# Optimization experiments

Measured on AMD Instinct MI355X. Metric: run time of the kernel, lower is better.

The kernel has to match this reference:

```python
import jax, jax.numpy as jnp
import numpy as np

D_MODEL = 1024
HEAD_SIZE = 128
SCALE = float(np.sqrt(HEAD_SIZE))


def setup_inputs() -> dict:
    key = jax.random.key(0)
    kx, kq, kk, kv = jax.random.split(key, 4)
    B, T = 4, 4096
    x = jax.random.normal(kx, (B, T, D_MODEL), dtype=jnp.float32)
    # torch nn.Linear(d_model, head_size, bias=False) weight: [head_size, d_model]
    s = 1.0 / np.sqrt(D_MODEL)
    Wq = jax.random.uniform(kq, (HEAD_SIZE, D_MODEL), jnp.float32, -s, s)
    Wk = jax.random.uniform(kk, (HEAD_SIZE, D_MODEL), jnp.float32, -s, s)
    Wv = jax.random.uniform(kv, (HEAD_SIZE, D_MODEL), jnp.float32, -s, s)
    return {"x": x, "Wq": Wq, "Wk": Wk, "Wv": Wv}


def reference(x, Wq, Wk, Wv):
    B, T, C = x.shape
    q = jnp.einsum('btc,hc->bth', x, Wq)  # [B,T,hs]
    k = jnp.einsum('btc,hc->bth', x, Wk)
    v = jnp.einsum('btc,hc->bth', x, Wv)
    scores = jnp.einsum('bth,bsh->bts', q, k) / SCALE  # [B,T,T]
    causal = jnp.tril(jnp.ones((T, T), dtype=bool))
    scores = jnp.where(causal, scores, -jnp.inf)
    attn = jax.nn.softmax(scores, axis=-1)
    # dropout p=0.0 -> identity
    return jnp.einsum('bts,bsh->bth', attn, v)
```

## Files before the change

kernel.cpp:

```cpp
#include <hip/hip_runtime.h>


typedef __attribute__((ext_vector_type(8))) short short8;
typedef __attribute__((ext_vector_type(8))) unsigned short ushort8;
typedef __attribute__((ext_vector_type(4))) unsigned short ushort4v;
typedef __attribute__((ext_vector_type(4))) float f32x4;
typedef __attribute__((ext_vector_type(16))) float f32x16;
typedef __attribute__((ext_vector_type(4))) int int4v;
typedef unsigned int u32;
typedef unsigned short u16;

#define MFMA32(a, b, c) __builtin_amdgcn_mfma_f32_32x32x16_bf16((a), (b), (c), 0, 0, 0)
#define WAITVM0() asm volatile("s_waitcnt vmcnt(0)" ::: "memory")
#define NEG_INF (-1e30f)

__device__ __forceinline__ void gload16(const void* g, void* l) {
  __builtin_amdgcn_global_load_lds((const __attribute__((address_space(1))) u32*)g,
                                   (__attribute__((address_space(3))) u32*)l, 16, 0, 0);
}

__device__ __forceinline__ u16 f2bf(float f) {
  u32 u = __builtin_bit_cast(u32, f);
  u = u + 0x7FFFu + ((u >> 16) & 1u);
  return (u16)(u >> 16);
}

__device__ __forceinline__ u32 cvtpk(float lo, float hi) {
  u32 r;
  asm("v_cvt_pk_bf16_f32 %0, %1, %2" : "=v"(r) : "v"(lo), "v"(hi));
  return r;
}

__global__ __launch_bounds__(256) void wconv_kernel(const float* __restrict__ Wq,
                                                    const float* __restrict__ Wk,
                                                    const float* __restrict__ Wv,
                                                    u16* __restrict__ Wb) {
  int g = (blockIdx.x * 256 + threadIdx.x) * 8;
  const float* src;
  if (g < 131072)      src = Wq + g;
  else if (g < 262144) src = Wk + (g - 131072);
  else                 src = Wv + (g - 262144);
  float4 a = *(const float4*)src;
  float4 b = *(const float4*)(src + 4);
  ushort8 o;
  o[0] = f2bf(a.x); o[1] = f2bf(a.y); o[2] = f2bf(a.z); o[3] = f2bf(a.w);
  o[4] = f2bf(b.x); o[5] = f2bf(b.y); o[6] = f2bf(b.z); o[7] = f2bf(b.w);
  *(ushort8*)(Wb + g) = o;
}

#define QK_SCALE 0.127517446f

__global__ __launch_bounds__(512, 2) void qkv_proj_kernel(const float* __restrict__ x,
                                                          const u16* __restrict__ Wb,
                                                          u16* __restrict__ qout,
                                                          u16* __restrict__ kout,
                                                          u16* __restrict__ vtout) {
  __shared__ __align__(16) unsigned char Wlds[2][49152];
  __shared__ __align__(16) unsigned char Xlds[2][8192];
  const int tid = threadIdx.x;
  const int w = tid >> 6;
  const int l = tid & 63;
  const int h = l >> 5, n32 = l & 31;
  const int mh = w >> 2, ng = w & 3;
  const int m0 = (int)blockIdx.x * 64;

  const int xr = tid >> 3, xc = tid & 7;
  const float* xsrc = x + (size_t)(m0 + xr) * 1024 + xc * 8;
  unsigned char* const xw0 = (unsigned char*)Xlds[0] + xr * 128 + ((xc * 16) ^ ((xr & 7) << 4));
  unsigned char* const xw1 = (unsigned char*)Xlds[1] + xr * 128 + ((xc * 16) ^ ((xr & 7) << 4));

  f32x16 acc[3];
#pragma unroll
  for (int j = 0; j < 3; ++j)
#pragma unroll
    for (int r = 0; r < 16; ++r) acc[j][r] = 0.f;

#define STAGE_W(buf, ks)                                                       \
  {                                                                            \
    _Pragma("unroll") for (int c = 0; c < 6; ++c) {                            \
      int L = c * 512 + tid;                                                   \
      int row = L >> 3, chp = L & 7;                                           \
      int gch = chp ^ (row & 7);                                               \
      gload16((const char*)Wb + row * 2048 + (ks) * 128 + gch * 16,            \
              (unsigned char*)Wlds[buf] + c * 8192 + w * 1024);                \
    }                                                                          \
  }

  float4 xa = *(const float4*)(xsrc);
  float4 xb = *(const float4*)(xsrc + 4);
  STAGE_W(0, 0);

  const int am = mh * 32 + n32;
  const int asw = (am & 7) << 4;
  int cur = 0;

  for (int ks = 0; ks < 16; ++ks) {
    int4v xv;
    xv[0] = (int)cvtpk(xa.x, xa.y);
    xv[1] = (int)cvtpk(xa.z, xa.w);
    xv[2] = (int)cvtpk(xb.x, xb.y);
    xv[3] = (int)cvtpk(xb.z, xb.w);
    *(int4v*)(cur ? xw1 : xw0) = xv;
    __syncthreads();
    if (ks < 15) {
      xa = *(const float4*)(xsrc + (ks + 1) * 64);
      xb = *(const float4*)(xsrc + (ks + 1) * 64 + 4);
      STAGE_W(cur ^ 1, ks + 1);
    }
    const char* xb0 = (const char*)Xlds[cur];
    const char* wb0 = (const char*)Wlds[cur];
    __builtin_amdgcn_s_setprio(1);
#pragma unroll
    for (int k16 = 0; k16 < 4; ++k16) {
      short8 a = *(const short8*)(xb0 + am * 128 + ((k16 * 32 + h * 16) ^ asw));
#pragma unroll
      for (int j = 0; j < 3; ++j) {
        int nrow = (ng * 3 + j) * 32 + n32;
        short8 b = *(const short8*)(wb0 + nrow * 128 +
                                    ((k16 * 32 + h * 16) ^ ((nrow & 7) << 4)));
        acc[j] = MFMA32(a, b, acc[j]);
      }
    }
    __builtin_amdgcn_s_setprio(0);
    cur ^= 1;
  }
#undef STAGE_W

  const int m0e = m0 + mh * 32;
#pragma unroll
  for (int j = 0; j < 3; ++j) {
    int ti = ng * 3 + j;
    int gcol = ti * 32 + n32;
    if (ti < 4) {
#pragma unroll
      for (int r = 0; r < 16; ++r) {
        int row = m0e + (r & 3) + 8 * (r >> 2) + 4 * h;
        qout[(size_t)row * 128 + gcol] = f2bf(acc[j][r] * QK_SCALE);
      }
    } else if (ti < 8) {
#pragma unroll
      for (int r = 0; r < 16; ++r) {
        int row = m0e + (r & 3) + 8 * (r >> 2) + 4 * h;
        kout[(size_t)row * 128 + (gcol - 128)] = f2bf(acc[j][r]);
      }
    } else {
      int d = gcol - 256;
#pragma unroll
      for (int rq = 0; rq < 4; ++rq) {
        int t0 = m0e + rq * 8 + 4 * h;
        ushort4v o4;
#pragma unroll
        for (int i = 0; i < 4; ++i) o4[i] = f2bf(acc[j][rq * 4 + i]);
        *(ushort4v*)&vtout[(size_t)((t0 >> 12) * 128 + d) * 4096 + (t0 & 4095)] = o4;
      }
    }
  }
}

template <int NSPLIT>
__global__ __launch_bounds__(256, 2) void attn_kernel(const u16* __restrict__ qws,
                                                      const u16* __restrict__ kws,
                                                      const u16* __restrict__ vtws,
                                                      float* __restrict__ out,
                                                      float* __restrict__ opart,
                                                      float* __restrict__ mlpart) {
  __shared__ __align__(16) unsigned char Klds[2][16384];
  __shared__ __align__(16) unsigned char Vlds[2][16384];

  const int tid = threadIdx.x;
  const int w = tid >> 6;
  const int l = tid & 63;
  const int h = l >> 5, q32 = l & 31;
  const int bid = (int)blockIdx.x;
  const int sp = bid & (NSPLIT - 1);
  const int tb = bid / NSPLIT;
  const int bi = tb & 3;
  const int qt = 31 - (tb >> 2);
  const int q0w = qt * 128 + w * 32;
  const int grow = bi * 4096 + q0w + q32;
  const int qg = q0w + q32;

  const int nsteps = 2 * qt + 2;
  const int s_lo = (nsteps * sp) / NSPLIT;
  const int s_hi = (nsteps * (sp + 1)) / NSPLIT;

  if constexpr (NSPLIT > 1) {
    if (s_lo >= s_hi) {
      if (h == 0) {
        mlpart[sp * 16384 + grow] = NEG_INF;
        mlpart[NSPLIT * 16384 + sp * 16384 + grow] = 0.f;
      }
      return;
    }
  }

  short8 qf[8];
  const u16* qp = qws + (size_t)grow * 128 + h * 8;
#pragma unroll
  for (int ks = 0; ks < 8; ++ks) qf[ks] = *(const short8*)(qp + ks * 16);

  f32x16 ot[4];
#pragma unroll
  for (int dt = 0; dt < 4; ++dt)
#pragma unroll
    for (int r = 0; r < 16; ++r) ot[dt][r] = 0.f;
  float mreg = NEG_INF, lsum = 0.f;

  const char* kbatch = (const char*)kws + (size_t)bi * 4096 * 256;
  const char* vbatch = (const char*)vtws + (size_t)bi * 128 * 8192;

#define STAGE_KV(buf, kv0)                                                     \
  {                                                                            \
    _Pragma("unroll") for (int c = 0; c < 4; ++c) {                            \
      int L = c * 256 + tid;                                                   \
      int row = L >> 4, chp = L & 15;                                          \
      int gch = chp ^ (row & 7);                                               \
      gload16(kbatch + (size_t)((kv0) + row) * 256 + gch * 16,                 \
              (unsigned char*)Klds[buf] + c * 4096 + w * 1024);                \
    }                                                                          \
    _Pragma("unroll") for (int c = 0; c < 4; ++c) {                            \
      int L = c * 256 + tid;                                                   \
      int row = L >> 3, chp = L & 7;                                           \
      int gch = chp ^ (row & 7);                                               \
      gload16(vbatch + (size_t)row * 8192 + (size_t)(kv0) * 2 + gch * 16,      \
              (unsigned char*)Vlds[buf] + c * 4096 + w * 1024);                \
    }                                                                          \
  }

  STAGE_KV(0, s_lo * 64);
  int cur = 0;

  for (int s = s_lo; s < s_hi; ++s) {
    WAITVM0();
    __builtin_amdgcn_s_barrier();
    __builtin_amdgcn_sched_barrier(0);
    if (s + 1 < s_hi) STAGE_KV(cur ^ 1, (s + 1) * 64);
    const int kv0 = s * 64;
    const bool active = (kv0 <= q0w + 31);

    if (active) {
      f32x16 st0, st1;
#pragma unroll
      for (int r = 0; r < 16; ++r) { st0[r] = 0.f; st1[r] = 0.f; }
      const char* Kb = (const char*)Klds[cur];
      const int sw = (q32 & 7) << 4;
      __builtin_amdgcn_s_setprio(1);
#pragma unroll
      for (int ks = 0; ks < 8; ++ks) {
        int coff = ks * 32 + h * 16;
        short8 a0 = *(const short8*)(Kb + q32 * 256 + (coff ^ sw));
        st0 = MFMA32(a0, qf[ks], st0);
        short8 a1 = *(const short8*)(Kb + (32 + q32) * 256 + (coff ^ sw));
        st1 = MFMA32(a1, qf[ks], st1);
      }
      __builtin_amdgcn_s_setprio(0);

      if (kv0 + 63 > q0w) {
#pragma unroll
        for (int r = 0; r < 16; ++r) {
          int kvr = kv0 + (r & 3) + 8 * (r >> 2) + 4 * h;
          if (kvr > qg) st0[r] = NEG_INF;
          if (kvr + 32 > qg) st1[r] = NEG_INF;
        }
      }

      float tmax = st0[0];
#pragma unroll
      for (int r = 1; r < 16; ++r) tmax = fmaxf(tmax, st0[r]);
#pragma unroll
      for (int r = 0; r < 16; ++r) tmax = fmaxf(tmax, st1[r]);
      tmax = fmaxf(tmax, __shfl_xor(tmax, 32));
      if (!__all(tmax <= mreg + 8.0f)) {
        float mnew = fmaxf(mreg, tmax);
        float alpha = exp2f(mreg - mnew);
        lsum *= alpha;
#pragma unroll
        for (int dt = 0; dt < 4; ++dt)
#pragma unroll
          for (int r = 0; r < 16; ++r) ot[dt][r] *= alpha;
        mreg = mnew;
      }
      float rs = 0.f;
#pragma unroll
      for (int r = 0; r < 16; ++r) { st0[r] = exp2f(st0[r] - mreg); rs += st0[r]; }
#pragma unroll
      for (int r = 0; r < 16; ++r) { st1[r] = exp2f(st1[r] - mreg); rs += st1[r]; }
      rs += __shfl_xor(rs, 32);
      lsum += rs;

      const char* Vb = (const char*)Vlds[cur];
      __builtin_amdgcn_s_setprio(1);
#pragma unroll
      for (int t = 0; t < 4; ++t) {
        const f32x16& stt = (t < 2) ? st0 : st1;
        const int rb = (t & 1) * 8;
        u32 A0 = cvtpk(stt[rb + 0], stt[rb + 1]);
        u32 C0 = cvtpk(stt[rb + 2], stt[rb + 3]);
        u32 B0 = cvtpk(stt[rb + 4], stt[rb + 5]);
        u32 D0 = cvtpk(stt[rb + 6], stt[rb + 7]);
        u32 Ax = (u32)__shfl_xor((int)A0, 32);
        u32 Bx = (u32)__shfl_xor((int)B0, 32);
        u32 Cx = (u32)__shfl_xor((int)C0, 32);
        u32 Dx = (u32)__shfl_xor((int)D0, 32);
        int4v pbv;
        pbv[0] = (int)(h ? Bx : A0);
        pbv[1] = (int)(h ? Dx : C0);
        pbv[2] = (int)(h ? B0 : Ax);
        pbv[3] = (int)(h ? D0 : Cx);
        short8 pb = __builtin_bit_cast(short8, pbv);
#pragma unroll
        for (int dt = 0; dt < 4; ++dt) {
          int row = dt * 32 + q32;
          short8 va = *(const short8*)(Vb + row * 128 + ((t * 32 + h * 16) ^ sw));
          ot[dt] = MFMA32(va, pb, ot[dt]);
        }
      }
      __builtin_amdgcn_s_setprio(0);
    }
    cur ^= 1;
  }

  if constexpr (NSPLIT == 1) {
    float inv = 1.0f / lsum;
    float* ob = out + (size_t)grow * 128;
#pragma unroll
    for (int dt = 0; dt < 4; ++dt)
#pragma unroll
      for (int rq = 0; rq < 4; ++rq) {
        f32x4 v4;
#pragma unroll
        for (int i = 0; i < 4; ++i) v4[i] = ot[dt][rq * 4 + i] * inv;
        *(f32x4*)(ob + dt * 32 + rq * 8 + 4 * h) = v4;
      }
  } else {
    float* ob = opart + ((size_t)sp * 16384 + grow) * 128;
#pragma unroll
    for (int dt = 0; dt < 4; ++dt)
#pragma unroll
      for (int rq = 0; rq < 4; ++rq) {
        f32x4 v4;
#pragma unroll
        for (int i = 0; i < 4; ++i) v4[i] = ot[dt][rq * 4 + i];
        *(f32x4*)(ob + dt * 32 + rq * 8 + 4 * h) = v4;
      }
    if (h == 0) {
      mlpart[sp * 16384 + grow] = mreg;
      mlpart[NSPLIT * 16384 + sp * 16384 + grow] = lsum;
    }
  }
#undef STAGE_KV
}

__global__ __launch_bounds__(256) void combine_kernel(const float* __restrict__ opart,
                                                      const float* __restrict__ mlpart,
                                                      float* __restrict__ out) {
  int idx = blockIdx.x * 256 + threadIdx.x;
  int row = idx >> 7;
  float m0 = mlpart[row], m1 = mlpart[16384 + row];
  float m2 = mlpart[32768 + row], m3 = mlpart[49152 + row];
  float M = fmaxf(fmaxf(m0, m1), fmaxf(m2, m3));
  float s0 = exp2f(m0 - M), s1 = exp2f(m1 - M);
  float s2 = exp2f(m2 - M), s3 = exp2f(m3 - M);
  const float* lp = mlpart + 65536;
  float L = lp[row] * s0 + lp[16384 + row] * s1 + lp[32768 + row] * s2 + lp[49152 + row] * s3;
  size_t o = (size_t)idx;
  float O = opart[o] * s0 + opart[o + 2097152] * s1 +
            opart[o + 4194304] * s2 + opart[o + 6291456] * s3;
  out[o] = O / L;
}

extern "C" void kernel_launch(void* const* d_in, const int* in_sizes, int n_in,
                              void* d_out, int out_size, void* d_ws, size_t ws_size,
                              hipStream_t stream) {
  (void)in_sizes; (void)n_in; (void)out_size;
  const float* x  = (const float*)d_in[0];
  const float* Wq = (const float*)d_in[1];
  const float* Wk = (const float*)d_in[2];
  const float* Wv = (const float*)d_in[3];
  float* out = (float*)d_out;
  char* ws = (char*)d_ws;
  u16* qws  = (u16*)(ws);
  u16* kws  = (u16*)(ws + (4u << 20));
  u16* vtws = (u16*)(ws + (8u << 20));
  u16* Wb   = (u16*)(ws + (12u << 20));
  float* opart  = (float*)(ws + (13u << 20));
  float* mlpart = (float*)(ws + (47u << 20));

  wconv_kernel<<<dim3(192), dim3(256), 0, stream>>>(Wq, Wk, Wv, Wb);
  qkv_proj_kernel<<<dim3(256), dim3(512), 0, stream>>>(x, Wb, qws, kws, vtws);
  if (ws_size >= ((size_t)48 << 20)) {
    attn_kernel<4><<<dim3(512), dim3(256), 0, stream>>>(qws, kws, vtws, nullptr, opart, mlpart);
    combine_kernel<<<dim3(8192), dim3(256), 0, stream>>>(opart, mlpart, out);
  } else {
    attn_kernel<1><<<dim3(128), dim3(256), 0, stream>>>(qws, kws, vtws, out, nullptr, nullptr);
  }
}
```

Measured before the change: 91.69 us.

## Balance split-KV attention with fixed-size chunks per query tile

Replaces the fixed 4-way KV split per query tile with a flat list of 476 work items. Each item covers at most 10 KV steps, and a query tile gets more items the longer its causal range is. The goal is to cap the longest block's work so that the long diagonal tiles no longer dominate the tail of the launch. In exchange, the combine kernel must loop over a variable number of partials per row and recompute the item offsets, and more partial outputs are written to workspace.

```diff
diff --git a/kernel.cpp b/kernel.cpp
--- a/kernel.cpp
+++ b/kernel.cpp
@@ -13,6 +13,10 @@
 #define MFMA32(a, b, c) __builtin_amdgcn_mfma_f32_32x32x16_bf16((a), (b), (c), 0, 0, 0)
 #define WAITVM0() asm volatile("s_waitcnt vmcnt(0)" ::: "memory")
 #define NEG_INF (-1e30f)
+
+#define CHUNK 10
+#define PITEMS 119
+#define NITEMS 476
 
 __device__ __forceinline__ void gload16(const void* g, void* l) {
   __builtin_amdgcn_global_load_lds((const __attribute__((address_space(1))) u32*)g,
@@ -157,7 +161,7 @@
   }
 }
 
-template <int NSPLIT>
+template <bool SPLIT>
 __global__ __launch_bounds__(256, 2) void attn_kernel(const u16* __restrict__ qws,
                                                       const u16* __restrict__ kws,
                                                       const u16* __restrict__ vtws,
@@ -171,28 +175,37 @@
   const int w = tid >> 6;
   const int l = tid & 63;
   const int h = l >> 5, q32 = l & 31;
-  const int bid = (int)blockIdx.x;
-  const int sp = bid & (NSPLIT - 1);
-  const int tb = bid / NSPLIT;
-  const int bi = tb & 3;
-  const int qt = 31 - (tb >> 2);
+
+  int bi, qt, s_lo, s_hi, item;
+  if constexpr (SPLIT) {
+    item = (int)blockIdx.x;
+    bi = item / PITEMS;
+    int r = item - bi * PITEMS;
+    int base = 0;
+    qt = 0;
+    while (true) {
+      int cnt = (qt + 5) / 5;
+      if (r < base + cnt) { break; }
+      base += cnt;
+      ++qt;
+    }
+    int cc = r - base;
+    int nsteps = 2 * qt + 2;
+    s_lo = cc * CHUNK;
+    s_hi = (s_lo + CHUNK < nsteps) ? s_lo + CHUNK : nsteps;
+  } else {
+    item = 0;
+    int tb = (int)blockIdx.x;
+    bi = tb & 3;
+    qt = 31 - (tb >> 2);
+    s_lo = 0;
+    s_hi = 2 * qt + 2;
+  }
+
   const int q0w = qt * 128 + w * 32;
-  const int grow = bi * 4096 + q0w + q32;
   const int qg = q0w + q32;
-
-  const int nsteps = 2 * qt + 2;
-  const int s_lo = (nsteps * sp) / NSPLIT;
-  const int s_hi = (nsteps * (sp + 1)) / NSPLIT;
-
-  if constexpr (NSPLIT > 1) {
-    if (s_lo >= s_hi) {
-      if (h == 0) {
-        mlpart[sp * 16384 + grow] = NEG_INF;
-        mlpart[NSPLIT * 16384 + sp * 16384 + grow] = 0.f;
-      }
-      return;
-    }
-  }
+  const int grow = bi * 4096 + qg;
+  const int ql = w * 32 + q32;
 
   short8 qf[8];
   const u16* qp = qws + (size_t)grow * 128 + h * 8;
@@ -320,7 +333,7 @@
     cur ^= 1;
   }
 
-  if constexpr (NSPLIT == 1) {
+  if constexpr (!SPLIT) {
     float inv = 1.0f / lsum;
     float* ob = out + (size_t)grow * 128;
 #pragma unroll
@@ -333,7 +346,7 @@
         *(f32x4*)(ob + dt * 32 + rq * 8 + 4 * h) = v4;
       }
   } else {
-    float* ob = opart + ((size_t)sp * 16384 + grow) * 128;
+    float* ob = opart + (size_t)item * 16384 + (size_t)ql * 128;
 #pragma unroll
     for (int dt = 0; dt < 4; ++dt)
 #pragma unroll
@@ -344,8 +357,8 @@
         *(f32x4*)(ob + dt * 32 + rq * 8 + 4 * h) = v4;
       }
     if (h == 0) {
-      mlpart[sp * 16384 + grow] = mreg;
-      mlpart[NSPLIT * 16384 + sp * 16384 + grow] = lsum;
+      mlpart[item * 128 + ql] = mreg;
+      mlpart[NITEMS * 128 + item * 128 + ql] = lsum;
     }
   }
 #undef STAGE_KV
@@ -355,18 +368,27 @@
                                                       const float* __restrict__ mlpart,
                                                       float* __restrict__ out) {
   int idx = blockIdx.x * 256 + threadIdx.x;
-  int row = idx >> 7;
-  float m0 = mlpart[row], m1 = mlpart[16384 + row];
-  float m2 = mlpart[32768 + row], m3 = mlpart[49152 + row];
-  float M = fmaxf(fmaxf(m0, m1), fmaxf(m2, m3));
-  float s0 = exp2f(m0 - M), s1 = exp2f(m1 - M);
-  float s2 = exp2f(m2 - M), s3 = exp2f(m3 - M);
-  const float* lp = mlpart + 65536;
-  float L = lp[row] * s0 + lp[16384 + row] * s1 + lp[32768 + row] * s2 + lp[49152 + row] * s3;
-  size_t o = (size_t)idx;
-  float O = opart[o] * s0 + opart[o + 2097152] * s1 +
-            opart[o + 4194304] * s2 + opart[o + 6291456] * s3;
-  out[o] = O / L;
+  int row = idx >> 7, d = idx & 127;
+  int bi = row >> 12, lrow = row & 4095;
+  int qt = lrow >> 7, ql = lrow & 127;
+  int base = 0;
+#pragma unroll 1
+  for (int j = 0; j < qt; ++j) base += (j + 5) / 5;
+  int nspl = (qt + 5) / 5;
+  int it0 = bi * PITEMS + base;
+
+  float M = NEG_INF;
+#pragma unroll 1
+  for (int j = 0; j < nspl; ++j)
+    M = fmaxf(M, mlpart[(it0 + j) * 128 + ql]);
+  float L = 0.f, O = 0.f;
+#pragma unroll 1
+  for (int j = 0; j < nspl; ++j) {
+    float s = exp2f(mlpart[(it0 + j) * 128 + ql] - M);
+    L += mlpart[NITEMS * 128 + (it0 + j) * 128 + ql] * s;
+    O += opart[(size_t)(it0 + j) * 16384 + (size_t)ql * 128 + d] * s;
+  }
+  out[(size_t)row * 128 + d] = O / L;
 }
 
 extern "C" void kernel_launch(void* const* d_in, const int* in_sizes, int n_in,
@@ -389,9 +411,9 @@
   wconv_kernel<<<dim3(192), dim3(256), 0, stream>>>(Wq, Wk, Wv, Wb);
   qkv_proj_kernel<<<dim3(256), dim3(512), 0, stream>>>(x, Wb, qws, kws, vtws);
   if (ws_size >= ((size_t)48 << 20)) {
-    attn_kernel<4><<<dim3(512), dim3(256), 0, stream>>>(qws, kws, vtws, nullptr, opart, mlpart);
+    attn_kernel<true><<<dim3(NITEMS), dim3(256), 0, stream>>>(qws, kws, vtws, nullptr, opart, mlpart);
     combine_kernel<<<dim3(8192), dim3(256), 0, stream>>>(opart, mlpart, out);
   } else {
-    attn_kernel<1><<<dim3(128), dim3(256), 0, stream>>>(qws, kws, vtws, out, nullptr, nullptr);
-  }
-}
+    attn_kernel<false><<<dim3(128), dim3(256), 0, stream>>>(qws, kws, vtws, out, nullptr, nullptr);
+  }
+}
```

New measurement: 92.62 us. Within noise of the previous version (+1.0%).
